# Kernel optimization log

Measured on AMD Instinct MI355X. Metric: run time of the kernel, lower is better.

## Reference

```python
import jax, jax.numpy as jnp
import numpy as np

B, V, P, C_IN = 2, 40000, 32, 4
GRID_X, GRID_Y = 750, 750
HID, OUT = 64, 128
EPS = 1e-5


def _bn1d(x, g, b):
    # x: [N, C]; batch-norm in training mode (biased variance), like nn.BatchNorm1d
    m = x.mean(0)
    v = ((x - m) ** 2).mean(0)
    return (x - m) * jax.lax.rsqrt(v + EPS) * g + b


def _bn2d(x, g, b):
    # x: [B, C, H, W]
    m = x.mean((0, 2, 3), keepdims=True)
    v = ((x - m) ** 2).mean((0, 2, 3), keepdims=True)
    return (x - m) * jax.lax.rsqrt(v + EPS) * g[None, :, None, None] + b[None, :, None, None]


def _conv3x3(x, w, b):
    y = jax.lax.conv_general_dilated(x, w, (1, 1), 'SAME',
                                     dimension_numbers=('NCHW', 'OIHW', 'NCHW'))
    return y + b[None, :, None, None]


def _forward(voxels, num_points, coords,
             W1, b1, g1, be1, W2, b2, g2, be2,
             Wc1, bc1, gc1, bec1, Wc2, bc2, gc2, bec2, Wc3, bc3, gc3, bec3):
    # ---- PillarFeatureNet ----
    mask = (jnp.arange(P)[None, None, :] < num_points[:, :, None]).astype(voxels.dtype)[..., None]  # [B,V,P,1]
    pillar_sum = (voxels * mask).sum(2)                      # [B,V,C]
    pillar_count = jnp.clip(mask.sum(2), 1.0, None)          # [B,V,1]
    pillar_center = pillar_sum / pillar_count                # [B,V,C]
    center_offset = voxels[..., :3] - pillar_center[:, :, None, :3]   # [B,V,P,3]
    aug = jnp.concatenate([voxels, center_offset, center_offset], -1)  # [B,V,P,10]
    flat = aug.reshape(-1, aug.shape[-1])
    h = jax.nn.relu(_bn1d(flat @ W1 + b1, g1, be1))
    h = jax.nn.relu(_bn1d(h @ W2 + b2, g2, be2))
    feats = h.reshape(B, V, P, HID) * mask                   # zero padded slots
    pillar_feats = feats.max(2)                              # [B,V,HID]

    # ---- PillarScatter (vectorized scatter, extra dummy row for out-of-range) ----
    x = coords[..., 0]
    y = coords[..., 1]
    valid = (x >= 0) & (x < GRID_X) & (y >= 0) & (y < GRID_Y)
    idx = jnp.where(valid, y * GRID_X + x, GRID_Y * GRID_X)  # [B,V]
    bev = jnp.zeros((B, GRID_Y * GRID_X + 1, HID), voxels.dtype)
    bev = bev.at[jnp.arange(B)[:, None], idx].set(pillar_feats)
    bev = bev[:, :-1].reshape(B, GRID_Y, GRID_X, HID).transpose(0, 3, 1, 2)  # [B,HID,Y,X]

    # ---- Backbone ----
    h = jax.nn.relu(_bn2d(_conv3x3(bev, Wc1, bc1), gc1, bec1))
    h = jax.nn.relu(_bn2d(_conv3x3(h, Wc2, bc2), gc2, bec2))
    h = jax.nn.relu(_bn2d(_conv3x3(h, Wc3, bc3), gc3, bec3))
    return h  # [B,OUT,Y,X]


def setup_inputs() -> dict:
    key = jax.random.key(0)
    ks = jax.random.split(key, 16)
    voxels = jax.random.normal(ks[0], (B, V, P, C_IN), jnp.float32)
    num_points = jax.random.randint(ks[1], (B, V), 0, P)
    # collision-free coords per batch so scatter 'set' is deterministic
    def mk_coords(k):
        h = jax.random.permutation(k, GRID_X * GRID_Y)[:V]
        return jnp.stack([h % GRID_X, h // GRID_X, jnp.zeros_like(h)], -1)
    coords = jnp.stack([mk_coords(ks[2]), mk_coords(ks[3])]).astype(jnp.int32)
    s = 0.05
    inp = dict(voxels=voxels, num_points=num_points, coords=coords,
               W1=jax.random.normal(ks[4], (10, HID)) * s, b1=jnp.zeros(HID),
               g1=jnp.ones(HID), be1=jnp.zeros(HID),
               W2=jax.random.normal(ks[5], (HID, HID)) * s, b2=jnp.zeros(HID),
               g2=jnp.ones(HID), be2=jnp.zeros(HID),
               Wc1=jax.random.normal(ks[6], (HID, HID, 3, 3)) * s, bc1=jnp.zeros(HID),
               gc1=jnp.ones(HID), bec1=jnp.zeros(HID),
               Wc2=jax.random.normal(ks[7], (HID, HID, 3, 3)) * s, bc2=jnp.zeros(HID),
               gc2=jnp.ones(HID), bec2=jnp.zeros(HID),
               Wc3=jax.random.normal(ks[8], (OUT, HID, 3, 3)) * s, bc3=jnp.zeros(OUT),
               gc3=jnp.ones(OUT), bec3=jnp.zeros(OUT))
    return inp


def reference(voxels, num_points, coords,
              W1, b1, g1, be1, W2, b2, g2, be2,
              Wc1, bc1, gc1, bec1, Wc2, bc2, gc2, bec2, Wc3, bc3, gc3, bec3):
    return _forward(voxels, num_points, coords,
                    W1, b1, g1, be1, W2, b2, g2, be2,
                    Wc1, bc1, gc1, bec1, Wc2, bc2, gc2, bec2, Wc3, bc3, gc3, bec3)
```

## Files before the change

kernel.cpp:

```cpp
#include <hip/hip_runtime.h>

#define BATCH 2
#define NV 40000
#define NPTS 32
#define GXX 750
#define GYY 750
#define HWSZ (GXX*GYY)
#define HIDC 64
#define OUTCH 128
#define NROWS (BATCH*NV*NPTS)
#define NBHW (BATCH*HWSZ)
#define EPSB 1e-5f

#define OFF_CENTER 0
#define OFF_STATS1 240000
#define OFF_AC1    240128
#define OFF_STATS2 240256
#define OFF_AC2    240384
#define OFF_SC1    240512
#define OFF_ACC1   240640
#define OFF_SC2    240768
#define OFF_ACC2   240896
#define OFF_SC3    241024
#define OFF_ACC3   241280
#define OFF_STATS_END 241536
#define OFF_WB1    241536
#define OFF_WB2    259968
#define OFF_WB3    278400
#define OFF_BEV    327680
#define OFF_MID    36327680

typedef __attribute__((ext_vector_type(8))) short bfrag8;
typedef __attribute__((ext_vector_type(4))) float f32x4;

__device__ __forceinline__ ushort f2bf(float f) {
    union { float f; unsigned u; } v; v.f = f;
    unsigned u = v.u;
    return (ushort)((u + 0x7FFFu + ((u >> 16) & 1u)) >> 16);
}

__global__ __launch_bounds__(256) void k_center(const float* __restrict__ vox,
                                                const int* __restrict__ npts,
                                                float* __restrict__ center) {
    int i = blockIdx.x * 256 + threadIdx.x;
    if (i >= BATCH * NV) return;
    int np = npts[i];
    if (np < 0) np = 0;
    if (np > NPTS) np = NPTS;
    const float* vp = vox + (size_t)i * (NPTS * 4);
    float sx = 0.f, sy = 0.f, sz = 0.f;
    for (int p = 0; p < np; ++p) {
        sx += vp[p * 4 + 0];
        sy += vp[p * 4 + 1];
        sz += vp[p * 4 + 2];
    }
    float cnt = np > 0 ? (float)np : 1.0f;
    center[i * 3 + 0] = sx / cnt;
    center[i * 3 + 1] = sy / cnt;
    center[i * 3 + 2] = sz / cnt;
}

__global__ __launch_bounds__(256) void k_fc1_stats(const float* __restrict__ vox,
                                                   const float* __restrict__ center,
                                                   const float* __restrict__ W1,
                                                   const float* __restrict__ b1,
                                                   float* __restrict__ stats) {
    __shared__ float sAug[64][12];
    __shared__ float red[2][4][64];
    const int t = threadIdx.x;
    const int c = t & 63, g = t >> 6;
    float w1c[10];
#pragma unroll
    for (int k = 0; k < 10; ++k) w1c[k] = W1[k * 64 + c];
    const float b1c = b1[c];
    float s0 = 0.f, s1 = 0.f;
    for (int tile = blockIdx.x; tile < NROWS / 64; tile += gridDim.x) {
        __syncthreads();
        if (t < 64) {
            int row = tile * 64 + t;
            int pil = row >> 5;
            float4 v = *(const float4*)(vox + (size_t)row * 4);
            float cx = center[pil * 3 + 0];
            float cy = center[pil * 3 + 1];
            float cz = center[pil * 3 + 2];
            sAug[t][0] = v.x; sAug[t][1] = v.y; sAug[t][2] = v.z; sAug[t][3] = v.w;
            sAug[t][4] = v.x - cx; sAug[t][5] = v.y - cy; sAug[t][6] = v.z - cz;
            sAug[t][7] = v.x - cx; sAug[t][8] = v.y - cy; sAug[t][9] = v.z - cz;
        }
        __syncthreads();
        for (int r = g; r < 64; r += 4) {
            float y = b1c;
#pragma unroll
            for (int k = 0; k < 10; ++k) y += sAug[r][k] * w1c[k];
            s0 += y;
            s1 += y * y;
        }
    }
    __syncthreads();
    red[0][g][c] = s0;
    red[1][g][c] = s1;
    __syncthreads();
    if (t < 64) {
        float a = red[0][0][t] + red[0][1][t] + red[0][2][t] + red[0][3][t];
        float b = red[1][0][t] + red[1][1][t] + red[1][2][t] + red[1][3][t];
        atomicAdd(&stats[t], a);
        atomicAdd(&stats[64 + t], b);
    }
}

__global__ void k_finalize(const float* __restrict__ stats,
                           const float* __restrict__ gamma,
                           const float* __restrict__ beta,
                           float* __restrict__ ac, int nch, float invN) {
    int c = blockIdx.x * blockDim.x + threadIdx.x;
    if (c >= nch) return;
    float m = stats[c] * invN;
    float v = stats[nch + c] * invN - m * m;
    if (v < 0.f) v = 0.f;
    float a = gamma[c] * rsqrtf(v + EPSB);
    ac[c] = a;
    ac[nch + c] = beta[c] - m * a;
}

__global__ __launch_bounds__(256) void k_fc2_stats(const float* __restrict__ vox,
                                                   const float* __restrict__ center,
                                                   const float* __restrict__ W1,
                                                   const float* __restrict__ b1,
                                                   const float* __restrict__ ac1,
                                                   const float* __restrict__ W2,
                                                   const float* __restrict__ b2,
                                                   float* __restrict__ stats) {
    __shared__ float sAug[64][12];
    __shared__ float sH[64][68];
    __shared__ float red[2][4][64];
    const int t = threadIdx.x;
    const int c = t & 63, g = t >> 6;
    float w1c[10];
#pragma unroll
    for (int k = 0; k < 10; ++k) w1c[k] = W1[k * 64 + c];
    float w2c[64];
#pragma unroll
    for (int k = 0; k < 64; ++k) w2c[k] = W2[k * 64 + c];
    const float b1c = b1[c];
    const float a1 = ac1[c], c1 = ac1[64 + c];
    const float b2c = b2[c];
    float s0 = 0.f, s1 = 0.f;
    for (int tile = blockIdx.x; tile < NROWS / 64; tile += gridDim.x) {
        __syncthreads();
        if (t < 64) {
            int row = tile * 64 + t;
            int pil = row >> 5;
            float4 v = *(const float4*)(vox + (size_t)row * 4);
            float cx = center[pil * 3 + 0];
            float cy = center[pil * 3 + 1];
            float cz = center[pil * 3 + 2];
            sAug[t][0] = v.x; sAug[t][1] = v.y; sAug[t][2] = v.z; sAug[t][3] = v.w;
            sAug[t][4] = v.x - cx; sAug[t][5] = v.y - cy; sAug[t][6] = v.z - cz;
            sAug[t][7] = v.x - cx; sAug[t][8] = v.y - cy; sAug[t][9] = v.z - cz;
        }
        __syncthreads();
        for (int r = g; r < 64; r += 4) {
            float y = b1c;
#pragma unroll
            for (int k = 0; k < 10; ++k) y += sAug[r][k] * w1c[k];
            y = a1 * y + c1;
            sH[r][c] = y > 0.f ? y : 0.f;
        }
        __syncthreads();
        for (int r = g; r < 64; r += 4) {
            float y = b2c;
#pragma unroll
            for (int k = 0; k < 64; k += 4) {
                float4 h = *(const float4*)&sH[r][k];
                y += h.x * w2c[k] + h.y * w2c[k + 1] + h.z * w2c[k + 2] + h.w * w2c[k + 3];
            }
            s0 += y;
            s1 += y * y;
        }
    }
    __syncthreads();
    red[0][g][c] = s0;
    red[1][g][c] = s1;
    __syncthreads();
    if (t < 64) {
        float a = red[0][0][t] + red[0][1][t] + red[0][2][t] + red[0][3][t];
        float b = red[1][0][t] + red[1][1][t] + red[1][2][t] + red[1][3][t];
        atomicAdd(&stats[t], a);
        atomicAdd(&stats[64 + t], b);
    }
}

__global__ __launch_bounds__(256) void k_pillar(const float* __restrict__ vox,
                                                const int* __restrict__ npts,
                                                const int* __restrict__ coords,
                                                const float* __restrict__ center,
                                                const float* __restrict__ W1,
                                                const float* __restrict__ b1,
                                                const float* __restrict__ ac1,
                                                const float* __restrict__ W2,
                                                const float* __restrict__ b2,
                                                const float* __restrict__ ac2,
                                                ushort* __restrict__ bev) {
    __shared__ float sAug[32][12];
    __shared__ float sH[32][68];
    __shared__ float red[4][64];
    const int t = threadIdx.x;
    const int c = t & 63, g = t >> 6;
    float w1c[10];
#pragma unroll
    for (int k = 0; k < 10; ++k) w1c[k] = W1[k * 64 + c];
    float w2c[64];
#pragma unroll
    for (int k = 0; k < 64; ++k) w2c[k] = W2[k * 64 + c];
    const float b1c = b1[c];
    const float a1 = ac1[c], c1 = ac1[64 + c];
    const float b2c = b2[c];
    const float a2 = ac2[c], c2 = ac2[64 + c];

    for (int pil = blockIdx.x; pil < BATCH * NV; pil += gridDim.x) {
        __syncthreads();
        int np = npts[pil];
        if (np < 0) np = 0;
        if (np > NPTS) np = NPTS;
        if (t < 32) {
            int row = pil * 32 + t;
            float4 v = *(const float4*)(vox + (size_t)row * 4);
            float cx = center[pil * 3 + 0];
            float cy = center[pil * 3 + 1];
            float cz = center[pil * 3 + 2];
            sAug[t][0] = v.x; sAug[t][1] = v.y; sAug[t][2] = v.z; sAug[t][3] = v.w;
            sAug[t][4] = v.x - cx; sAug[t][5] = v.y - cy; sAug[t][6] = v.z - cz;
            sAug[t][7] = v.x - cx; sAug[t][8] = v.y - cy; sAug[t][9] = v.z - cz;
        }
        __syncthreads();
        for (int p = g; p < np; p += 4) {
            float y = b1c;
#pragma unroll
            for (int k = 0; k < 10; ++k) y += sAug[p][k] * w1c[k];
            y = a1 * y + c1;
            sH[p][c] = y > 0.f ? y : 0.f;
        }
        __syncthreads();
        float mx = 0.f;
        for (int p = g; p < np; p += 4) {
            float y = b2c;
#pragma unroll
            for (int k = 0; k < 64; k += 4) {
                float4 h = *(const float4*)&sH[p][k];
                y += h.x * w2c[k] + h.y * w2c[k + 1] + h.z * w2c[k + 2] + h.w * w2c[k + 3];
            }
            y = a2 * y + c2;
            if (y > mx) mx = y;
        }
        red[g][c] = mx;
        __syncthreads();
        if (t < 64) {
            float m0 = red[0][t] > red[1][t] ? red[0][t] : red[1][t];
            float m1 = red[2][t] > red[3][t] ? red[2][t] : red[3][t];
            float m = m0 > m1 ? m0 : m1;
            int x = coords[pil * 3 + 0];
            int y = coords[pil * 3 + 1];
            if (x >= 0 && x < GXX && y >= 0 && y < GYY) {
                int b = pil / NV;
                bev[((size_t)((b * GYY + y) * GXX + x)) * 64 + t] = f2bf(m);
            }
        }
    }
}

__global__ __launch_bounds__(256) void k_wcvt(const float* __restrict__ src,
                                              ushort* __restrict__ dst, int OC) {
    int idx = blockIdx.x * 256 + threadIdx.x;
    if (idx >= OC * 64 * 9) return;
    int oc = idx / 576;
    int rem = idx - oc * 576;
    int ic = rem / 9;
    int tp = rem - ic * 9;
    dst[((size_t)(tp * OC + oc)) * 64 + ic] = f2bf(src[idx]);
}

#define ICP 72
__global__ __launch_bounds__(256) void k_conv_mfma(const ushort* __restrict__ in,
                                                   const ushort* __restrict__ Wb,
                                                   const float* __restrict__ bias,
                                                   const float* __restrict__ acIn,
                                                   int useAffine,
                                                   float* __restrict__ outF,
                                                   ushort* __restrict__ outH,
                                                   int N,
                                                   float* __restrict__ stats) {
    __shared__ ushort sX[18 * 18 * ICP];
    __shared__ float sStat[2][4][64];
    const int t = threadIdx.x;
    const int wid = t >> 6, l = t & 63;
    const int hi = l >> 4, lr = l & 15;
    const int tilex = blockIdx.x % 47, tiley = blockIdx.x / 47;
    const int x0 = tilex * 16, y0 = tiley * 16;
    const int ocb = blockIdx.y * 64;
    const int b = blockIdx.z;

    const int c8 = t & 7;
    float aA[8], aC[8];
    if (useAffine) {
#pragma unroll
        for (int i = 0; i < 8; ++i) { aA[i] = acIn[c8 * 8 + i]; aC[i] = acIn[64 + c8 * 8 + i]; }
    }
    for (int idx = t; idx < 18 * 18 * 8; idx += 256) {
        int pix = idx >> 3;
        int r = pix / 18, cpx = pix - r * 18;
        int gy = y0 + r - 1, gx = x0 + cpx - 1;
        uint4 v = {0u, 0u, 0u, 0u};
        if (gy >= 0 && gy < GYY && gx >= 0 && gx < GXX) {
            v = *(const uint4*)(in + ((size_t)((b * GYY + gy) * GXX + gx)) * 64 + c8 * 8);
            if (useAffine) {
                uint uu[4] = {v.x, v.y, v.z, v.w};
#pragma unroll
                for (int p = 0; p < 4; ++p) {
                    float f0 = __uint_as_float(uu[p] << 16);
                    float f1 = __uint_as_float(uu[p] & 0xFFFF0000u);
                    f0 = fmaxf(fmaf(aA[p * 2], f0, aC[p * 2]), 0.f);
                    f1 = fmaxf(fmaf(aA[p * 2 + 1], f1, aC[p * 2 + 1]), 0.f);
                    uu[p] = (uint)f2bf(f0) | ((uint)f2bf(f1) << 16);
                }
                v.x = uu[0]; v.y = uu[1]; v.z = uu[2]; v.w = uu[3];
            }
        }
        *(uint4*)(&sX[pix * ICP + ((c8 ^ (pix & 7)) << 3)]) = v;
    }
    __syncthreads();

    f32x4 acc[4][4];
#pragma unroll
    for (int m = 0; m < 4; ++m)
#pragma unroll
        for (int n = 0; n < 4; ++n) acc[m][n] = (f32x4){0.f, 0.f, 0.f, 0.f};

    const int yb = wid * 4;
    for (int tp = 0; tp < 9; ++tp) {
        const int dy = tp / 3 - 1, dx = tp % 3 - 1;
#pragma unroll
        for (int kb = 0; kb < 2; ++kb) {
            bfrag8 w[4];
#pragma unroll
            for (int n = 0; n < 4; ++n)
                w[n] = *(const bfrag8*)(Wb + ((size_t)(tp * N + ocb + n * 16 + lr)) * 64 + kb * 32 + hi * 8);
            const int kc = kb * 4 + hi;
#pragma unroll
            for (int m = 0; m < 4; ++m) {
                int pix = (yb + m + 1 + dy) * 18 + (lr + 1 + dx);
                bfrag8 a = *(const bfrag8*)(&sX[pix * ICP + ((kc ^ (pix & 7)) << 3)]);
#pragma unroll
                for (int n = 0; n < 4; ++n)
                    acc[m][n] = __builtin_amdgcn_mfma_f32_16x16x32_bf16(a, w[n], acc[m][n], 0, 0, 0);
            }
        }
    }

    float ssum[4] = {0.f, 0.f, 0.f, 0.f}, ssq[4] = {0.f, 0.f, 0.f, 0.f};
#pragma unroll
    for (int n = 0; n < 4; ++n) {
        const int oc = ocb + n * 16 + lr;
        const float bo = bias[oc];
#pragma unroll
        for (int m = 0; m < 4; ++m) {
            int y = y0 + yb + m;
            if (y < GYY) {
#pragma unroll
                for (int j = 0; j < 4; ++j) {
                    int x = x0 + hi * 4 + j;
                    if (x < GXX) {
                        float v = acc[m][n][j] + bo;
                        if (outH) outH[((size_t)((b * GYY + y) * GXX + x)) * 64 + oc] = f2bf(v);
                        else outF[((size_t)(b * N + oc)) * HWSZ + (size_t)y * GXX + x] = v;
                        ssum[n] += v;
                        ssq[n] += v * v;
                    }
                }
            }
        }
    }
#pragma unroll
    for (int n = 0; n < 4; ++n) {
        ssum[n] += __shfl_xor(ssum[n], 16);
        ssum[n] += __shfl_xor(ssum[n], 32);
        ssq[n] += __shfl_xor(ssq[n], 16);
        ssq[n] += __shfl_xor(ssq[n], 32);
    }
    if (l < 16) {
#pragma unroll
        for (int n = 0; n < 4; ++n) {
            sStat[0][wid][n * 16 + l] = ssum[n];
            sStat[1][wid][n * 16 + l] = ssq[n];
        }
    }
    __syncthreads();
    if (t < 64) {
        float s = sStat[0][0][t] + sStat[0][1][t] + sStat[0][2][t] + sStat[0][3][t];
        float q = sStat[1][0][t] + sStat[1][1][t] + sStat[1][2][t] + sStat[1][3][t];
        atomicAdd(&stats[ocb + t], s);
        atomicAdd(&stats[N + ocb + t], q);
    }
}

__global__ __launch_bounds__(256) void k_bnrelu(float* __restrict__ x,
                                                const float* __restrict__ ac, int nch) {
    const int hw4 = HWSZ / 4;
    size_t total = (size_t)BATCH * nch * hw4;
    size_t stride = (size_t)gridDim.x * 256;
    for (size_t idx = (size_t)blockIdx.x * 256 + threadIdx.x; idx < total; idx += stride) {
        int c = (int)((idx / hw4) % nch);
        float a = ac[c], cc = ac[nch + c];
        float4 v = ((float4*)x)[idx];
        v.x = fmaxf(a * v.x + cc, 0.f);
        v.y = fmaxf(a * v.y + cc, 0.f);
        v.z = fmaxf(a * v.z + cc, 0.f);
        v.w = fmaxf(a * v.w + cc, 0.f);
        ((float4*)x)[idx] = v;
    }
}

extern "C" void kernel_launch(void* const* d_in, const int* in_sizes, int n_in,
                              void* d_out, int out_size, void* d_ws, size_t ws_size,
                              hipStream_t stream) {
    const float* voxels = (const float*)d_in[0];
    const int* num_points = (const int*)d_in[1];
    const int* coords = (const int*)d_in[2];
    const float* W1 = (const float*)d_in[3];
    const float* b1 = (const float*)d_in[4];
    const float* g1 = (const float*)d_in[5];
    const float* be1 = (const float*)d_in[6];
    const float* W2 = (const float*)d_in[7];
    const float* b2 = (const float*)d_in[8];
    const float* g2 = (const float*)d_in[9];
    const float* be2 = (const float*)d_in[10];
    const float* Wc1 = (const float*)d_in[11];
    const float* bc1 = (const float*)d_in[12];
    const float* gc1 = (const float*)d_in[13];
    const float* bec1 = (const float*)d_in[14];
    const float* Wc2 = (const float*)d_in[15];
    const float* bc2 = (const float*)d_in[16];
    const float* gc2 = (const float*)d_in[17];
    const float* bec2 = (const float*)d_in[18];
    const float* Wc3 = (const float*)d_in[19];
    const float* bc3 = (const float*)d_in[20];
    const float* gc3 = (const float*)d_in[21];
    const float* bec3 = (const float*)d_in[22];

    float* ws = (float*)d_ws;
    float* center = ws + OFF_CENTER;
    float* stats1 = ws + OFF_STATS1;
    float* ac1 = ws + OFF_AC1;
    float* stats2 = ws + OFF_STATS2;
    float* ac2 = ws + OFF_AC2;
    float* sC1 = ws + OFF_SC1;
    float* acC1 = ws + OFF_ACC1;
    float* sC2 = ws + OFF_SC2;
    float* acC2 = ws + OFF_ACC2;
    float* sC3 = ws + OFF_SC3;
    float* acC3 = ws + OFF_ACC3;
    ushort* Wb1 = (ushort*)(ws + OFF_WB1);
    ushort* Wb2 = (ushort*)(ws + OFF_WB2);
    ushort* Wb3 = (ushort*)(ws + OFF_WB3);
    ushort* bev = (ushort*)(ws + OFF_BEV);
    ushort* mid = (ushort*)(ws + OFF_MID);
    float* outf = (float*)d_out;

    hipMemsetAsync((char*)d_ws + OFF_STATS1 * sizeof(float), 0,
                   (OFF_STATS_END - OFF_STATS1) * sizeof(float), stream);
    hipMemsetAsync((char*)d_ws + OFF_BEV * sizeof(float), 0,
                   (size_t)BATCH * HWSZ * 64 * sizeof(ushort), stream);

    k_wcvt<<<144, 256, 0, stream>>>(Wc1, Wb1, 64);
    k_wcvt<<<144, 256, 0, stream>>>(Wc2, Wb2, 64);
    k_wcvt<<<288, 256, 0, stream>>>(Wc3, Wb3, 128);

    k_center<<<(BATCH * NV + 255) / 256, 256, 0, stream>>>(voxels, num_points, center);

    k_fc1_stats<<<1024, 256, 0, stream>>>(voxels, center, W1, b1, stats1);
    k_finalize<<<1, 64, 0, stream>>>(stats1, g1, be1, ac1, 64, 1.0f / NROWS);

    k_fc2_stats<<<1024, 256, 0, stream>>>(voxels, center, W1, b1, ac1, W2, b2, stats2);
    k_finalize<<<1, 64, 0, stream>>>(stats2, g2, be2, ac2, 64, 1.0f / NROWS);

    k_pillar<<<4096, 256, 0, stream>>>(voxels, num_points, coords, center,
                                       W1, b1, ac1, W2, b2, ac2, bev);

    const int NT = 47 * 47;
    {
        dim3 grid(NT, 1, BATCH);
        k_conv_mfma<<<grid, 256, 0, stream>>>(bev, Wb1, bc1, nullptr, 0,
                                              nullptr, mid, 64, sC1);
        k_finalize<<<1, 64, 0, stream>>>(sC1, gc1, bec1, acC1, 64, 1.0f / NBHW);
    }
    {
        dim3 grid(NT, 1, BATCH);
        k_conv_mfma<<<grid, 256, 0, stream>>>(mid, Wb2, bc2, acC1, 1,
                                              nullptr, bev, 64, sC2);
        k_finalize<<<1, 64, 0, stream>>>(sC2, gc2, bec2, acC2, 64, 1.0f / NBHW);
    }
    {
        dim3 grid(NT, 2, BATCH);
        k_conv_mfma<<<grid, 256, 0, stream>>>(bev, Wb3, bc3, acC2, 1,
                                              outf, nullptr, 128, sC3);
        k_finalize<<<1, 128, 0, stream>>>(sC3, gc3, bec3, acC3, 128, 1.0f / NBHW);
    }
    k_bnrelu<<<4096, 256, 0, stream>>>(outf, acC3, 128);
}
```

Before: 3.331 ms.

## Split conv input-channel staging into two halves and preload all tap weights

The 3x3 MFMA conv now stages the input tile in two passes of 32 channels each, with a smaller LDS row pitch (40 instead of 72) and no XOR swizzle. All 9 taps' weight fragments for a pass are preloaded into registers. Launch bounds now request 2 blocks per CU. This cuts LDS footprint and weight reload latency inside the tap loop, but adds an extra sync/load phase and more register pressure, and may reintroduce LDS bank conflicts without the swizzle.

```diff
diff --git a/kernel.cpp b/kernel.cpp
--- a/kernel.cpp
+++ b/kernel.cpp
@@ -279,17 +279,17 @@
     dst[((size_t)(tp * OC + oc)) * 64 + ic] = f2bf(src[idx]);
 }
 
-#define ICP 72
-__global__ __launch_bounds__(256) void k_conv_mfma(const ushort* __restrict__ in,
-                                                   const ushort* __restrict__ Wb,
-                                                   const float* __restrict__ bias,
-                                                   const float* __restrict__ acIn,
-                                                   int useAffine,
-                                                   float* __restrict__ outF,
-                                                   ushort* __restrict__ outH,
-                                                   int N,
-                                                   float* __restrict__ stats) {
-    __shared__ ushort sX[18 * 18 * ICP];
+#define ICP2 40
+__global__ __launch_bounds__(256, 2) void k_conv_mfma(const ushort* __restrict__ in,
+                                                      const ushort* __restrict__ Wb,
+                                                      const float* __restrict__ bias,
+                                                      const float* __restrict__ acIn,
+                                                      int useAffine,
+                                                      float* __restrict__ outF,
+                                                      ushort* __restrict__ outH,
+                                                      int N,
+                                                      float* __restrict__ stats) {
+    __shared__ ushort sX[18 * 18 * ICP2];
     __shared__ float sStat[2][4][64];
     const int t = threadIdx.x;
     const int wid = t >> 6, l = t & 63;
@@ -298,60 +298,67 @@
     const int x0 = tilex * 16, y0 = tiley * 16;
     const int ocb = blockIdx.y * 64;
     const int b = blockIdx.z;
-
-    const int c8 = t & 7;
-    float aA[8], aC[8];
-    if (useAffine) {
-#pragma unroll
-        for (int i = 0; i < 8; ++i) { aA[i] = acIn[c8 * 8 + i]; aC[i] = acIn[64 + c8 * 8 + i]; }
-    }
-    for (int idx = t; idx < 18 * 18 * 8; idx += 256) {
-        int pix = idx >> 3;
-        int r = pix / 18, cpx = pix - r * 18;
-        int gy = y0 + r - 1, gx = x0 + cpx - 1;
-        uint4 v = {0u, 0u, 0u, 0u};
-        if (gy >= 0 && gy < GYY && gx >= 0 && gx < GXX) {
-            v = *(const uint4*)(in + ((size_t)((b * GYY + gy) * GXX + gx)) * 64 + c8 * 8);
-            if (useAffine) {
-                uint uu[4] = {v.x, v.y, v.z, v.w};
-#pragma unroll
-                for (int p = 0; p < 4; ++p) {
-                    float f0 = __uint_as_float(uu[p] << 16);
-                    float f1 = __uint_as_float(uu[p] & 0xFFFF0000u);
-                    f0 = fmaxf(fmaf(aA[p * 2], f0, aC[p * 2]), 0.f);
-                    f1 = fmaxf(fmaf(aA[p * 2 + 1], f1, aC[p * 2 + 1]), 0.f);
-                    uu[p] = (uint)f2bf(f0) | ((uint)f2bf(f1) << 16);
+    const int cch = t & 3;
+    const int px0 = t >> 2;
+
+    f32x4 acc[4][4];
+#pragma unroll
+    for (int m = 0; m < 4; ++m)
+#pragma unroll
+        for (int n = 0; n < 4; ++n) acc[m][n] = (f32x4){0.f, 0.f, 0.f, 0.f};
+
+#pragma unroll
+    for (int pass = 0; pass < 2; ++pass) {
+        __syncthreads();
+        bfrag8 w[9][4];
+#pragma unroll
+        for (int tp = 0; tp < 9; ++tp)
+#pragma unroll
+            for (int n = 0; n < 4; ++n)
+                w[tp][n] = *(const bfrag8*)(Wb + ((size_t)(tp * N + ocb + n * 16 + lr)) * 64
+                                            + pass * 32 + hi * 8);
+        float aA[8], aC[8];
+        if (useAffine) {
+#pragma unroll
+            for (int i = 0; i < 8; ++i) {
+                aA[i] = acIn[pass * 32 + cch * 8 + i];
+                aC[i] = acIn[64 + pass * 32 + cch * 8 + i];
+            }
+        }
+        for (int pix = px0; pix < 324; pix += 64) {
+            int r = pix / 18, cpx = pix - r * 18;
+            int gy = y0 + r - 1, gx = x0 + cpx - 1;
+            uint4 v = {0u, 0u, 0u, 0u};
+            if (gy >= 0 && gy < GYY && gx >= 0 && gx < GXX) {
+                v = *(const uint4*)(in + ((size_t)((b * GYY + gy) * GXX + gx)) * 64
+                                    + pass * 32 + cch * 8);
+                if (useAffine) {
+                    uint uu[4] = {v.x, v.y, v.z, v.w};
+#pragma unroll
+                    for (int p = 0; p < 4; ++p) {
+                        float f0 = __uint_as_float(uu[p] << 16);
+                        float f1 = __uint_as_float(uu[p] & 0xFFFF0000u);
+                        f0 = fmaxf(fmaf(aA[p * 2], f0, aC[p * 2]), 0.f);
+                        f1 = fmaxf(fmaf(aA[p * 2 + 1], f1, aC[p * 2 + 1]), 0.f);
+                        uu[p] = (uint)f2bf(f0) | ((uint)f2bf(f1) << 16);
+                    }
+                    v.x = uu[0]; v.y = uu[1]; v.z = uu[2]; v.w = uu[3];
                 }
-                v.x = uu[0]; v.y = uu[1]; v.z = uu[2]; v.w = uu[3];
-            }
-        }
-        *(uint4*)(&sX[pix * ICP + ((c8 ^ (pix & 7)) << 3)]) = v;
-    }
-    __syncthreads();
-
-    f32x4 acc[4][4];
-#pragma unroll
-    for (int m = 0; m < 4; ++m)
-#pragma unroll
-        for (int n = 0; n < 4; ++n) acc[m][n] = (f32x4){0.f, 0.f, 0.f, 0.f};
-
-    const int yb = wid * 4;
-    for (int tp = 0; tp < 9; ++tp) {
-        const int dy = tp / 3 - 1, dx = tp % 3 - 1;
-#pragma unroll
-        for (int kb = 0; kb < 2; ++kb) {
-            bfrag8 w[4];
-#pragma unroll
-            for (int n = 0; n < 4; ++n)
-                w[n] = *(const bfrag8*)(Wb + ((size_t)(tp * N + ocb + n * 16 + lr)) * 64 + kb * 32 + hi * 8);
-            const int kc = kb * 4 + hi;
+            }
+            *(uint4*)(&sX[pix * ICP2 + cch * 8]) = v;
+        }
+        __syncthreads();
+        const int yb = wid * 4;
+#pragma unroll
+        for (int tp = 0; tp < 9; ++tp) {
+            const int dy = tp / 3 - 1, dx = tp % 3 - 1;
 #pragma unroll
             for (int m = 0; m < 4; ++m) {
                 int pix = (yb + m + 1 + dy) * 18 + (lr + 1 + dx);
-                bfrag8 a = *(const bfrag8*)(&sX[pix * ICP + ((kc ^ (pix & 7)) << 3)]);
+                bfrag8 a = *(const bfrag8*)(&sX[pix * ICP2 + hi * 8]);
 #pragma unroll
                 for (int n = 0; n < 4; ++n)
-                    acc[m][n] = __builtin_amdgcn_mfma_f32_16x16x32_bf16(a, w[n], acc[m][n], 0, 0, 0);
+                    acc[m][n] = __builtin_amdgcn_mfma_f32_16x16x32_bf16(a, w[tp][n], acc[m][n], 0, 0, 0);
             }
         }
     }
@@ -363,7 +370,7 @@
         const float bo = bias[oc];
 #pragma unroll
         for (int m = 0; m < 4; ++m) {
-            int y = y0 + yb + m;
+            int y = y0 + wid * 4 + m;
             if (y < GYY) {
 #pragma unroll
                 for (int j = 0; j < 4; ++j) {
```

Result: slower. 3.740 ms (+12.3%).

## Stage conv weights in double-buffered LDS and vectorize fp32 output stores

Applied to the files above, without the earlier changes.

The conv kernel now copies each tap's 64x64 bf16 weight slice into a padded, double-buffered LDS array, prefetching the next tap while computing the current one. Weight fragments are read from LDS instead of global memory. The XOR swizzle on the input tile is removed and replaced by plain padding. Interior tiles write fp32 output as float4. This adds one block barrier per tap and reuses the weight buffer for the stats reduction.

```diff
diff --git a/kernel.cpp b/kernel.cpp
--- a/kernel.cpp
+++ b/kernel.cpp
@@ -280,6 +280,7 @@
 }
 
 #define ICP 72
+#define WPAD 72
 __global__ __launch_bounds__(256) void k_conv_mfma(const ushort* __restrict__ in,
                                                    const ushort* __restrict__ Wb,
                                                    const float* __restrict__ bias,
@@ -289,8 +290,10 @@
                                                    ushort* __restrict__ outH,
                                                    int N,
                                                    float* __restrict__ stats) {
-    __shared__ ushort sX[18 * 18 * ICP];
-    __shared__ float sStat[2][4][64];
+    __shared__ __align__(16) ushort sX[324 * ICP];
+    __shared__ __align__(16) ushort sW[2][64 * WPAD];
+    float* sStat = (float*)&sW[0][0];
+
     const int t = threadIdx.x;
     const int wid = t >> 6, l = t & 63;
     const int hi = l >> 4, lr = l & 15;
@@ -298,14 +301,14 @@
     const int x0 = tilex * 16, y0 = tiley * 16;
     const int ocb = blockIdx.y * 64;
     const int b = blockIdx.z;
-
     const int c8 = t & 7;
+
     float aA[8], aC[8];
     if (useAffine) {
 #pragma unroll
         for (int i = 0; i < 8; ++i) { aA[i] = acIn[c8 * 8 + i]; aC[i] = acIn[64 + c8 * 8 + i]; }
     }
-    for (int idx = t; idx < 18 * 18 * 8; idx += 256) {
+    for (int idx = t; idx < 324 * 8; idx += 256) {
         int pix = idx >> 3;
         int r = pix / 18, cpx = pix - r * 18;
         int gy = y0 + r - 1, gx = x0 + cpx - 1;
@@ -325,7 +328,17 @@
                 v.x = uu[0]; v.y = uu[1]; v.z = uu[2]; v.w = uu[3];
             }
         }
-        *(uint4*)(&sX[pix * ICP + ((c8 ^ (pix & 7)) << 3)]) = v;
+        *(uint4*)(&sX[pix * ICP + c8 * 8]) = v;
+    }
+    {
+        const ushort* src = Wb + (size_t)(0 * N + ocb) * 64;
+#pragma unroll
+        for (int k = 0; k < 2; ++k) {
+            int idx = t + k * 256;
+            int oc = idx >> 3, ch = idx & 7;
+            uint4 v = *(const uint4*)(src + oc * 64 + ch * 8);
+            *(uint4*)(&sW[0][oc * WPAD + ch * 8]) = v;
+        }
     }
     __syncthreads();
 
@@ -335,45 +348,82 @@
 #pragma unroll
         for (int n = 0; n < 4; ++n) acc[m][n] = (f32x4){0.f, 0.f, 0.f, 0.f};
 
-    const int yb = wid * 4;
     for (int tp = 0; tp < 9; ++tp) {
+        if (tp < 8) {
+            const ushort* src = Wb + (size_t)((tp + 1) * N + ocb) * 64;
+            ushort* dst = sW[(tp + 1) & 1];
+#pragma unroll
+            for (int k = 0; k < 2; ++k) {
+                int idx = t + k * 256;
+                int oc = idx >> 3, ch = idx & 7;
+                uint4 v = *(const uint4*)(src + oc * 64 + ch * 8);
+                *(uint4*)(&dst[oc * WPAD + ch * 8]) = v;
+            }
+        }
+        const ushort* wbuf = sW[tp & 1];
         const int dy = tp / 3 - 1, dx = tp % 3 - 1;
+        const int rowb = (wid * 4 + 1 + dy) * 18 + (lr + 1 + dx);
 #pragma unroll
         for (int kb = 0; kb < 2; ++kb) {
+            const int kc = kb * 4 + hi;
             bfrag8 w[4];
 #pragma unroll
             for (int n = 0; n < 4; ++n)
-                w[n] = *(const bfrag8*)(Wb + ((size_t)(tp * N + ocb + n * 16 + lr)) * 64 + kb * 32 + hi * 8);
-            const int kc = kb * 4 + hi;
+                w[n] = *(const bfrag8*)(&wbuf[(n * 16 + lr) * WPAD + kc * 8]);
 #pragma unroll
             for (int m = 0; m < 4; ++m) {
-                int pix = (yb + m + 1 + dy) * 18 + (lr + 1 + dx);
-                bfrag8 a = *(const bfrag8*)(&sX[pix * ICP + ((kc ^ (pix & 7)) << 3)]);
+                bfrag8 a = *(const bfrag8*)(&sX[(rowb + m * 18) * ICP + kc * 8]);
 #pragma unroll
                 for (int n = 0; n < 4; ++n)
                     acc[m][n] = __builtin_amdgcn_mfma_f32_16x16x32_bf16(a, w[n], acc[m][n], 0, 0, 0);
             }
         }
+        __syncthreads();
     }
 
     float ssum[4] = {0.f, 0.f, 0.f, 0.f}, ssq[4] = {0.f, 0.f, 0.f, 0.f};
+    const bool fullx = (x0 + 15 < GXX);
 #pragma unroll
     for (int n = 0; n < 4; ++n) {
         const int oc = ocb + n * 16 + lr;
         const float bo = bias[oc];
 #pragma unroll
         for (int m = 0; m < 4; ++m) {
-            int y = y0 + yb + m;
+            int y = y0 + wid * 4 + m;
             if (y < GYY) {
-#pragma unroll
-                for (int j = 0; j < 4; ++j) {
-                    int x = x0 + hi * 4 + j;
-                    if (x < GXX) {
-                        float v = acc[m][n][j] + bo;
-                        if (outH) outH[((size_t)((b * GYY + y) * GXX + x)) * 64 + oc] = f2bf(v);
-                        else outF[((size_t)(b * N + oc)) * HWSZ + (size_t)y * GXX + x] = v;
-                        ssum[n] += v;
-                        ssq[n] += v * v;
+                float4 v4;
+                v4.x = acc[m][n][0] + bo;
+                v4.y = acc[m][n][1] + bo;
+                v4.z = acc[m][n][2] + bo;
+                v4.w = acc[m][n][3] + bo;
+                if (outF) {
+                    size_t base = ((size_t)(b * N + oc)) * HWSZ + (size_t)y * GXX + x0 + hi * 4;
+                    if (fullx) {
+                        *(float4*)(outF + base) = v4;
+                        ssum[n] += v4.x + v4.y + v4.z + v4.w;
+                        ssq[n] += v4.x * v4.x + v4.y * v4.y + v4.z * v4.z + v4.w * v4.w;
+                    } else {
+                        float vv[4] = {v4.x, v4.y, v4.z, v4.w};
+#pragma unroll
+                        for (int j = 0; j < 4; ++j) {
+                            int x = x0 + hi * 4 + j;
+                            if (x < GXX) {
+                                outF[base + j] = vv[j];
+                                ssum[n] += vv[j];
+                                ssq[n] += vv[j] * vv[j];
+                            }
+                        }
+                    }
+                } else {
+                    float vv[4] = {v4.x, v4.y, v4.z, v4.w};
+#pragma unroll
+                    for (int j = 0; j < 4; ++j) {
+                        int x = x0 + hi * 4 + j;
+                        if (x < GXX) {
+                            outH[((size_t)((b * GYY + y) * GXX + x)) * 64 + oc] = f2bf(vv[j]);
+                            ssum[n] += vv[j];
+                            ssq[n] += vv[j] * vv[j];
+                        }
                     }
                 }
             }
@@ -386,17 +436,18 @@
         ssq[n] += __shfl_xor(ssq[n], 16);
         ssq[n] += __shfl_xor(ssq[n], 32);
     }
+    __syncthreads();
     if (l < 16) {
 #pragma unroll
         for (int n = 0; n < 4; ++n) {
-            sStat[0][wid][n * 16 + l] = ssum[n];
-            sStat[1][wid][n * 16 + l] = ssq[n];
+            sStat[(0 * 4 + wid) * 64 + n * 16 + l] = ssum[n];
+            sStat[(1 * 4 + wid) * 64 + n * 16 + l] = ssq[n];
         }
     }
     __syncthreads();
     if (t < 64) {
-        float s = sStat[0][0][t] + sStat[0][1][t] + sStat[0][2][t] + sStat[0][3][t];
-        float q = sStat[1][0][t] + sStat[1][1][t] + sStat[1][2][t] + sStat[1][3][t];
+        float s = sStat[0 * 64 + t] + sStat[1 * 64 + t] + sStat[2 * 64 + t] + sStat[3 * 64 + t];
+        float q = sStat[4 * 64 + t] + sStat[5 * 64 + t] + sStat[6 * 64 + t] + sStat[7 * 64 + t];
         atomicAdd(&stats[ocb + t], s);
         atomicAdd(&stats[N + ocb + t], q);
     }
```

Measured after the change: 2.783 ms. 16.5% less time.
